# Optimization experiments

Hardware: AMD Instinct MI355X
Metric: run time of the kernel (lower is better)

## Reference

```python
import jax, jax.numpy as jnp
import numpy as np

HIDDEN = 1024
NUM_EXPERTS = 16
TOP_K = 2
I_TEXT = 512
I_VISION = 256
NUM_SHARED = 2
NORM_MIN = 1e-12


def _sparse_moe(x, router_w, bias, gate_up, down):
    """One Ernie4_5_VLMoeSparseMoeBlock applied to flat tokens x: [T, H].

    router_w: [E, H], bias: [E] (e_score_correction_bias),
    gate_up: [E, H, 2I], down: [E, I, H].
    Returns (y [T, H], router_logits [T, E]).
    """
    T = x.shape[0]
    # fp32 router (torch runs it with autocast disabled in float32)
    logits = x @ router_w.T                                  # [T, E]
    probs = jax.nn.softmax(logits, axis=-1)
    # top-k on bias-corrected probs, but gather the *uncorrected* probs
    _, sel = jax.lax.top_k(probs + bias[None, :], TOP_K)     # [T, k]
    w = jnp.take_along_axis(probs, sel, axis=1)              # [T, k]
    w = w / jnp.maximum(jnp.sum(w, axis=-1, keepdims=True), NORM_MIN)
    # sparse combine matrix [T, E] with k nonzeros per row
    combine = jnp.zeros((T, NUM_EXPERTS), x.dtype).at[
        jnp.arange(T)[:, None], sel].add(w)
    # batched per-expert gated-SiLU MLP (dense dispatch reference)
    gu = jnp.einsum('th,ehi->eti', x, gate_up)               # [E, T, 2I]
    g, u = jnp.split(gu, 2, axis=-1)
    h = jnp.einsum('eti,eih->eth', jax.nn.silu(g) * u, down)  # [E, T, H]
    y = jnp.einsum('te,eth->th', combine, h)                 # [T, H]
    return y, logits


def setup_inputs() -> dict:
    key = jax.random.key(0)
    ks = jax.random.split(key, 16)
    s = 0.02
    B, S = 1, 1024
    return {
        'hidden_states': jax.random.normal(ks[0], (B, S, HIDDEN), jnp.float32),
        'moe_mm_token_type_ids': jax.random.randint(ks[1], (B, S), 0, 2).astype(jnp.int32),
        'text_router_weight': s * jax.random.normal(ks[2], (NUM_EXPERTS, HIDDEN), jnp.float32),
        'text_bias': s * jax.random.normal(ks[3], (NUM_EXPERTS,), jnp.float32),
        'text_gate_up': s * jax.random.normal(ks[4], (NUM_EXPERTS, HIDDEN, 2 * I_TEXT), jnp.float32),
        'text_down': s * jax.random.normal(ks[5], (NUM_EXPERTS, I_TEXT, HIDDEN), jnp.float32),
        'vision_router_weight': s * jax.random.normal(ks[6], (NUM_EXPERTS, HIDDEN), jnp.float32),
        'vision_bias': s * jax.random.normal(ks[7], (NUM_EXPERTS,), jnp.float32),
        'vision_gate_up': s * jax.random.normal(ks[8], (NUM_EXPERTS, HIDDEN, 2 * I_VISION), jnp.float32),
        'vision_down': s * jax.random.normal(ks[9], (NUM_EXPERTS, I_VISION, HIDDEN), jnp.float32),
        'shared_gate': s * jax.random.normal(ks[10], (HIDDEN, NUM_SHARED * I_TEXT), jnp.float32),
        'shared_up': s * jax.random.normal(ks[11], (HIDDEN, NUM_SHARED * I_TEXT), jnp.float32),
        'shared_down': s * jax.random.normal(ks[12], (NUM_SHARED * I_TEXT, HIDDEN), jnp.float32),
    }


def reference(hidden_states, moe_mm_token_type_ids,
              text_router_weight, text_bias, text_gate_up, text_down,
              vision_router_weight, vision_bias, vision_gate_up, vision_down,
              shared_gate, shared_up, shared_down):
    B, S, H = hidden_states.shape
    x = hidden_states.reshape(-1, H)                         # [T, H]
    # shared experts MLP (gated SiLU) on all tokens
    shared = (jax.nn.silu(x @ shared_gate) * (x @ shared_up)) @ shared_down
    # modality-isolated MoEs; each is pointwise-per-token, so running both on
    # all tokens and selecting with the mask is math-equivalent to the
    # boolean-mask dispatch in the torch code (jit-friendly, no dynamic shapes)
    y_text, lg_text = _sparse_moe(x, text_router_weight, text_bias, text_gate_up, text_down)
    y_vis, lg_vis = _sparse_moe(x, vision_router_weight, vision_bias, vision_gate_up, vision_down)
    is_vision = (moe_mm_token_type_ids.reshape(-1) != 0)[:, None]  # [T, 1]
    final = jnp.where(is_vision, y_vis, y_text) + shared
    router_logits = jnp.where(is_vision, lg_vis, lg_text)    # [T, E]
    return final.reshape(B, S, H), router_logits
```

## Files before the change

### kernel.cpp

```cpp
#include <hip/hip_runtime.h>
#include <math.h>

#define TOK  1024
#define HID  1024
#define NEXP 16

typedef __attribute__((ext_vector_type(8))) short bf16x8;
typedef __attribute__((ext_vector_type(4))) float f32x4;

#define SW_GUT 0u
#define SW_GUV 16777216u
#define SW_DNT 25165824u
#define SW_DNV 33554432u
#define SW_SG  37748736u
#define SW_SU  38797312u
#define SW_SD  39845888u
#define SW_ELEMS 40894464ull
#define WS_SMALL 6554624ull
#define WS_FAST (WS_SMALL + SW_ELEMS * 2ull)

__device__ __forceinline__ unsigned pack2(float f0, float f1) {
    union { float f; unsigned u; } a, b; a.f = f0; b.f = f1;
    return __builtin_amdgcn_perm(b.u + 0x8000u, a.u + 0x8000u, 0x07060302u);
}
__device__ __forceinline__ unsigned short f2bf(float f) {
    union { float f; unsigned u; } v; v.f = f;
    return (unsigned short)((v.u + 0x8000u) >> 16);
}
__device__ __forceinline__ f32x4 ntload4(const float* p) {
    return __builtin_nontemporal_load((const f32x4*)p);
}

__global__ void k_init(float* __restrict__ out, int* __restrict__ counts) {
    size_t i = (size_t)blockIdx.x * blockDim.x + threadIdx.x;
    ((float4*)out)[i] = make_float4(0.f, 0.f, 0.f, 0.f);
    if (blockIdx.x == 0 && threadIdx.x < 32) counts[threadIdx.x] = 0;
}

__global__ __launch_bounds__(64)
void k_router(const float* __restrict__ x, const int* __restrict__ tt,
              const float* __restrict__ rw_t, const float* __restrict__ b_t,
              const float* __restrict__ rw_v, const float* __restrict__ b_v,
              float* __restrict__ out_logits,
              int* __restrict__ counts, int* __restrict__ lists,
              float* __restrict__ wlist, unsigned short* __restrict__ Xbf)
{
    const int t = blockIdx.x;
    const int lane = threadIdx.x;
    const bool vis = (tt[t] != 0);
    const float* rw   = vis ? rw_v : rw_t;
    const float* bias = vis ? b_v  : b_t;
    const float* xr = x + (size_t)t * HID;

#pragma unroll
    for (int jj = 0; jj < 2; ++jj) {
        int j0 = jj * 512 + lane * 8;
        float4 lo = *(const float4*)(xr + j0);
        float4 hi = *(const float4*)(xr + j0 + 4);
        union { bf16x8 v; unsigned d[4]; } u;
        u.d[0] = pack2(lo.x, lo.y); u.d[1] = pack2(lo.z, lo.w);
        u.d[2] = pack2(hi.x, hi.y); u.d[3] = pack2(hi.z, hi.w);
        *(bf16x8*)(Xbf + (size_t)t * HID + j0) = u.v;
    }

    float acc[NEXP];
#pragma unroll
    for (int e = 0; e < NEXP; ++e) acc[e] = 0.f;
    for (int j = 0; j < HID; j += 64) {
        const float xv = xr[j + lane];
#pragma unroll
        for (int e = 0; e < NEXP; ++e)
            acc[e] = fmaf(xv, rw[(size_t)e * HID + j + lane], acc[e]);
    }
#pragma unroll
    for (int e = 0; e < NEXP; ++e) {
        float v = acc[e];
#pragma unroll
        for (int off = 32; off; off >>= 1) v += __shfl_xor(v, off);
        acc[e] = v;
    }
    if (lane < NEXP) out_logits[(size_t)t * NEXP + lane] = acc[lane];

    if (lane == 0) {
        float mx = acc[0];
#pragma unroll
        for (int e = 1; e < NEXP; ++e) mx = fmaxf(mx, acc[e]);
        float p[NEXP], s = 0.f;
#pragma unroll
        for (int e = 0; e < NEXP; ++e) { p[e] = expf(acc[e] - mx); s += p[e]; }
        const float inv = 1.f / s;
#pragma unroll
        for (int e = 0; e < NEXP; ++e) p[e] *= inv;

        int s1 = 0; float v1 = p[0] + bias[0];
#pragma unroll
        for (int e = 1; e < NEXP; ++e) {
            float c = p[e] + bias[e];
            if (c > v1) { v1 = c; s1 = e; }
        }
        int s2 = -1; float v2 = -1e30f;
#pragma unroll
        for (int e = 0; e < NEXP; ++e) {
            if (e == s1) continue;
            float c = p[e] + bias[e];
            if (c > v2) { v2 = c; s2 = e; }
        }
        float w1 = p[s1], w2 = p[s2];
        float sw = fmaxf(w1 + w2, 1e-12f);
        w1 /= sw; w2 /= sw;

        const int base = vis ? NEXP : 0;
        int pos1 = atomicAdd(&counts[base + s1], 1);
        lists[(base + s1) * TOK + pos1] = t * 2 + 0;
        wlist[(base + s1) * TOK + pos1] = w1;
        int pos2 = atomicAdd(&counts[base + s2], 1);
        lists[(base + s2) * TOK + pos2] = t * 2 + 1;
        wlist[(base + s2) * TOK + pos2] = w2;
    }
}

__device__ __forceinline__ void conv_decode(
    int bid,
    const float* gut, const float* guv, const float* dnt, const float* dnv,
    const float* sg, const float* su, const float* sd, unsigned short* sw,
    const float*& src, unsigned short*& dst, int& K, int& N, int& c, int& p)
{
    if (bid < 2048)      { int i = bid;        int e = i >> 7, r = i & 127; c = r >> 2; p = r & 3; K = 1024; N = 1024; src = gut + (size_t)e * 1048576; dst = sw + SW_GUT + (size_t)e * 1048576; }
    else if (bid < 3072) { int i = bid - 2048; int e = i >> 6, r = i & 63;  c = r >> 1; p = r & 1; K = 1024; N = 512;  src = guv + (size_t)e * 524288;  dst = sw + SW_GUV + (size_t)e * 524288; }
    else if (bid < 4096) { int i = bid - 3072; int e = i >> 6, r = i & 63;  c = r >> 2; p = r & 3; K = 512;  N = 1024; src = dnt + (size_t)e * 524288;  dst = sw + SW_DNT + (size_t)e * 524288; }
    else if (bid < 4608) { int i = bid - 4096; int e = i >> 5, r = i & 31;  c = r >> 2; p = r & 3; K = 256;  N = 1024; src = dnv + (size_t)e * 262144;  dst = sw + SW_DNV + (size_t)e * 262144; }
    else if (bid < 4736) { int i = bid - 4608; c = i >> 2; p = i & 3; K = 1024; N = 1024; src = sg; dst = sw + SW_SG; }
    else if (bid < 4864) { int i = bid - 4736; c = i >> 2; p = i & 3; K = 1024; N = 1024; src = su; dst = sw + SW_SU; }
    else                 { int i = bid - 4864; c = i >> 2; p = i & 3; K = 1024; N = 1024; src = sd; dst = sw + SW_SD; }
}

__global__ __launch_bounds__(256)
void k_conv(const float* __restrict__ gut, const float* __restrict__ guv,
            const float* __restrict__ dnt, const float* __restrict__ dnv,
            const float* __restrict__ sg, const float* __restrict__ su,
            const float* __restrict__ sd, unsigned short* __restrict__ sw)
{
    __shared__ unsigned ls[16 * 258];
    const int tid = threadIdx.x;
    const int b0 = blockIdx.x * 2;

    const float *sA, *sB; unsigned short *dA, *dB;
    int KA, NA, cA, pA, KB, NB, cB, pB;
    conv_decode(b0 + 0, gut, guv, dnt, dnv, sg, su, sd, sw, sA, dA, KA, NA, cA, pA);
    conv_decode(b0 + 1, gut, guv, dnt, dnv, sg, su, sd, sw, sB, dB, KB, NB, cB, pB);

    f32x4 Ra[8], Rb[8];
#pragma unroll
    for (int i = 0; i < 4; ++i) {
        int u = tid + i * 256; int kp = u >> 6, c4 = u & 63;
        const float* r0 = sA + (size_t)(cA * 32 + 2 * kp) * NA + pA * 256 + c4 * 4;
        Ra[2 * i]     = ntload4(r0);
        Ra[2 * i + 1] = ntload4(r0 + NA);
    }
#pragma unroll
    for (int i = 0; i < 4; ++i) {
        int u = tid + i * 256; int kp = u >> 6, c4 = u & 63;
        const float* r0 = sB + (size_t)(cB * 32 + 2 * kp) * NB + pB * 256 + c4 * 4;
        Rb[2 * i]     = ntload4(r0);
        Rb[2 * i + 1] = ntload4(r0 + NB);
    }

#pragma unroll
    for (int i = 0; i < 4; ++i) {
        int u = tid + i * 256; int kp = u >> 6, c4 = u & 63;
        unsigned* lp = &ls[kp * 258 + c4 * 4];
        f32x4 a = Ra[2 * i], b = Ra[2 * i + 1];
        lp[0] = pack2(a[0], b[0]); lp[1] = pack2(a[1], b[1]);
        lp[2] = pack2(a[2], b[2]); lp[3] = pack2(a[3], b[3]);
    }
    __syncthreads();
    {
        const int KC = KA >> 5;
#pragma unroll
        for (int i = 0; i < 4; ++i) {
            int u = tid + i * 256;
            int tt = u >> 6, l = u & 63;
            int q = l >> 4, lm = l & 15;
            int col = tt * 16 + lm;
            unsigned d0 = ls[(q * 4 + 0) * 258 + col];
            unsigned d1 = ls[(q * 4 + 1) * 258 + col];
            unsigned d2 = ls[(q * 4 + 2) * 258 + col];
            unsigned d3 = ls[(q * 4 + 3) * 258 + col];
            size_t off = ((size_t)((pA * 16 + tt) * KC + cA) * 64 + l) * 8;
            *(uint4*)(dA + off) = make_uint4(d0, d1, d2, d3);
        }
    }
    __syncthreads();

#pragma unroll
    for (int i = 0; i < 4; ++i) {
        int u = tid + i * 256; int kp = u >> 6, c4 = u & 63;
        unsigned* lp = &ls[kp * 258 + c4 * 4];
        f32x4 a = Rb[2 * i], b = Rb[2 * i + 1];
        lp[0] = pack2(a[0], b[0]); lp[1] = pack2(a[1], b[1]);
        lp[2] = pack2(a[2], b[2]); lp[3] = pack2(a[3], b[3]);
    }
    __syncthreads();
    {
        const int KC = KB >> 5;
#pragma unroll
        for (int i = 0; i < 4; ++i) {
            int u = tid + i * 256;
            int tt = u >> 6, l = u & 63;
            int q = l >> 4, lm = l & 15;
            int col = tt * 16 + lm;
            unsigned d0 = ls[(q * 4 + 0) * 258 + col];
            unsigned d1 = ls[(q * 4 + 1) * 258 + col];
            unsigned d2 = ls[(q * 4 + 2) * 258 + col];
            unsigned d3 = ls[(q * 4 + 3) * 258 + col];
            size_t off = ((size_t)((pB * 16 + tt) * KC + cB) * 64 + l) * 8;
            *(uint4*)(dB + off) = make_uint4(d0, d1, d2, d3);
        }
    }
}

__global__ __launch_bounds__(256)
void k_gu2(const unsigned short* __restrict__ Xbf, const unsigned short* __restrict__ sw,
           const int* __restrict__ counts, const int* __restrict__ lists,
           unsigned short* __restrict__ hbuf, unsigned short* __restrict__ hsh)
{
    const int z = blockIdx.z;
    int M, I, utile0;
    const unsigned short *gbase, *ubase;
    if (z == 32)      { M = TOK;       I = 1024; gbase = sw + SW_SG; ubase = sw + SW_SU; utile0 = 0; }
    else if (z < 16)  { M = counts[z]; I = 512;  gbase = ubase = sw + SW_GUT + (size_t)z * 1048576; utile0 = 32; }
    else              { M = counts[z]; I = 256;  gbase = ubase = sw + SW_GUV + (size_t)(z - 16) * 524288; utile0 = 16; }
    const int xI = blockIdx.x * 16, m0 = blockIdx.y * 64;
    if (xI >= I || m0 >= M) return;

    __shared__ int s_aid[64];
    const int tid = threadIdx.x;
    if (tid < 64) {
        int r = m0 + tid;
        s_aid[tid] = (z == 32) ? r : ((r < M) ? lists[z * TOK + r] : -1);
    }
    __syncthreads();

    const int w = tid >> 6, lane = tid & 63;
    const int lm = lane & 15, q = lane >> 4;

    int aidA = s_aid[w * 16 + lm];
    int tr = (z == 32) ? aidA : (aidA < 0 ? 0 : (aidA >> 1));
    const unsigned short* arow = Xbf + (size_t)tr * HID;

    const int tg = xI >> 4;
    const int tu = utile0 + tg;
    const unsigned short* pg = gbase + (size_t)tg * 32 * 512 + lane * 8;
    const unsigned short* pu = ubase + (size_t)tu * 32 * 512 + lane * 8;
    const int ko = q * 8;

    f32x4 accG = {}, accU = {};
    bf16x8 Bg[4], Bu[4], Af[4];
#pragma unroll
    for (int p = 0; p < 4; ++p) {
        Bg[p] = *(const bf16x8*)(pg + p * 512);
        Bu[p] = *(const bf16x8*)(pu + p * 512);
        Af[p] = *(const bf16x8*)(arow + p * 32 + ko);
    }
    for (int cc = 0; cc < 32; cc += 4) {
#pragma unroll
        for (int p = 0; p < 4; ++p) {
            accG = __builtin_amdgcn_mfma_f32_16x16x32_bf16(Af[p], Bg[p], accG, 0, 0, 0);
            accU = __builtin_amdgcn_mfma_f32_16x16x32_bf16(Af[p], Bu[p], accU, 0, 0, 0);
            int cp = cc + p + 4; if (cp > 31) cp = 31;
            Bg[p] = *(const bf16x8*)(pg + cp * 512);
            Bu[p] = *(const bf16x8*)(pu + cp * 512);
            Af[p] = *(const bf16x8*)(arow + cp * 32 + ko);
        }
    }

    const int i = xI + lm;
#pragma unroll
    for (int r = 0; r < 4; ++r) {
        int row = w * 16 + q * 4 + r;
        int aid = s_aid[row];
        if (aid < 0) continue;
        float g = accG[r], uu = accU[r];
        float h = g / (1.f + __expf(-g)) * uu;
        if (z == 32) hsh[(size_t)aid * 1024 + i] = f2bf(h);
        else         hbuf[(size_t)aid * 512 + i] = f2bf(h);
    }
}

__global__ __launch_bounds__(256)
void k_down2(const unsigned short* __restrict__ hbuf, const unsigned short* __restrict__ hsh,
             const unsigned short* __restrict__ sw,
             const int* __restrict__ counts, const int* __restrict__ lists,
             const float* __restrict__ wlist, float* __restrict__ out)
{
    const int z = blockIdx.z;
    int M, K;
    const unsigned short* base;
    if (z == 32)     { M = TOK;       K = 1024; base = sw + SW_SD; }
    else if (z < 16) { M = counts[z]; K = 512;  base = sw + SW_DNT + (size_t)z * 524288; }
    else             { M = counts[z]; K = 256;  base = sw + SW_DNV + (size_t)(z - 16) * 262144; }
    const int n0 = blockIdx.x * 16, m0 = blockIdx.y * 64;
    if (m0 >= M) return;

    __shared__ int s_aid[64];
    __shared__ float s_w[64];
    const int tid = threadIdx.x;
    if (tid < 64) {
        int r = m0 + tid;
        if (z == 32)    { s_aid[tid] = r; s_w[tid] = 1.f; }
        else if (r < M) { s_aid[tid] = lists[z * TOK + r]; s_w[tid] = wlist[z * TOK + r]; }
        else            { s_aid[tid] = -1; s_w[tid] = 0.f; }
    }
    __syncthreads();

    const int w = tid >> 6, lane = tid & 63;
    const int lm = lane & 15, q = lane >> 4;

    int aidA = s_aid[w * 16 + lm];
    const unsigned short* hrow = (z == 32) ? (hsh + (size_t)aidA * 1024)
                                           : (hbuf + (size_t)(aidA < 0 ? 0 : aidA) * 512);

    const int KC = K >> 5;
    const int t = blockIdx.x;
    const unsigned short* pb = base + (size_t)t * KC * 512 + lane * 8;
    const int ko = q * 8;

    f32x4 acc = {};
    bf16x8 Bt[4], Af[4];
#pragma unroll
    for (int p = 0; p < 4; ++p) {
        Bt[p] = *(const bf16x8*)(pb + p * 512);
        Af[p] = *(const bf16x8*)(hrow + p * 32 + ko);
    }
    const int last = KC - 1;
    for (int cc = 0; cc < KC; cc += 4) {
#pragma unroll
        for (int p = 0; p < 4; ++p) {
            acc = __builtin_amdgcn_mfma_f32_16x16x32_bf16(Af[p], Bt[p], acc, 0, 0, 0);
            int cp = cc + p + 4; if (cp > last) cp = last;
            Bt[p] = *(const bf16x8*)(pb + (size_t)cp * 512);
            Af[p] = *(const bf16x8*)(hrow + cp * 32 + ko);
        }
    }

    const int col = n0 + lm;
#pragma unroll
    for (int r = 0; r < 4; ++r) {
        int row = w * 16 + q * 4 + r;
        int aid = s_aid[row];
        if (aid < 0) continue;
        int tok = (z == 32) ? aid : (aid >> 1);
        atomicAdd(&out[(size_t)tok * HID + col], s_w[row] * acc[r]);
    }
}

__global__ __launch_bounds__(256)
void k_gu_fb(const unsigned short* __restrict__ Xbf,
             const float* __restrict__ gut, const float* __restrict__ guv,
             const float* __restrict__ sg, const float* __restrict__ su,
             const int* __restrict__ counts, const int* __restrict__ lists,
             unsigned short* __restrict__ hbuf, unsigned short* __restrict__ hsh)
{
    const int z = blockIdx.z;
    int M, I, str;
    const float *Wg, *Wu;
    if (z == 32) { M = TOK; I = 1024; str = 1024; Wg = sg; Wu = su; }
    else {
        M = counts[z];
        const int mod = z >> 4, e = z & 15;
        I = mod ? 256 : 512; str = 2 * I;
        const float* base = mod ? (guv + (size_t)e * HID * 512)
                                : (gut + (size_t)e * HID * 1024);
        Wg = base; Wu = base + I;
    }
    const int xI = blockIdx.x * 64;
    const int m0 = blockIdx.y * 64;
    if (xI >= I || m0 >= M) return;

    __shared__ float bs[8192];
    __shared__ int s_aid[64];
    const int tid = threadIdx.x;
    const int wid = tid >> 6, lane = tid & 63;
    const int lm = lane & 15, q = lane >> 4;

    if (tid < 64) {
        int r = m0 + tid;
        s_aid[tid] = (z == 32) ? r : ((r < M) ? lists[z * TOK + r] : -1);
    }
    __syncthreads();

    const unsigned short* arow[4];
#pragma unroll
    for (int s = 0; s < 4; ++s) {
        int aid = s_aid[s * 16 + lm];
        int tr = (z == 32) ? aid : (aid < 0 ? 0 : (aid >> 1));
        arow[s] = Xbf + (size_t)tr * HID;
    }
    int urow[8], uc4[8], scell[8];
#pragma unroll
    for (int r = 0; r < 8; ++r) {
        int u = r * 256 + tid;
        int k = u >> 5;
        urow[r] = k; uc4[r] = u & 31;
        scell[r] = k * 32 + ((u & 31) ^ (((k >> 3) & 1) << 2));
    }
    int fidx[2];
#pragma unroll
    for (int reg = 0; reg < 2; ++reg) {
        int c = reg * 64 + wid * 16 + lm;
        fidx[reg] = (q * 8) * 128 + (((c >> 2) ^ ((q & 1) << 2)) * 4 + (c & 3));
    }
    float4 R[8];
#pragma unroll
    for (int r = 0; r < 8; ++r) {
        int c4 = uc4[r];
        const float* gp = (c4 < 16) ? (Wg + (size_t)urow[r] * str + xI + c4 * 4)
                                    : (Wu + (size_t)urow[r] * str + xI + (c4 - 16) * 4);
        R[r] = *(const float4*)gp;
    }
    f32x4 accG[4] = {}, accU[4] = {};
    for (int kc = 0; kc < 16; ++kc) {
        if (kc) __syncthreads();
#pragma unroll
        for (int r = 0; r < 8; ++r)
            *(float4*)&bs[scell[r] * 4] = R[r];
        __syncthreads();
        bf16x8 af[2][4];
        const int kg = kc * 64 + q * 8;
#pragma unroll
        for (int s = 0; s < 4; ++s) {
            af[0][s] = *(const bf16x8*)(arow[s] + kg);
            af[1][s] = *(const bf16x8*)(arow[s] + kg + 32);
        }
        if (kc + 1 < 16) {
            const int k0 = (kc + 1) * 64;
#pragma unroll
            for (int r = 0; r < 8; ++r) {
                int c4 = uc4[r];
                const float* gp = (c4 < 16) ? (Wg + (size_t)(k0 + urow[r]) * str + xI + c4 * 4)
                                            : (Wu + (size_t)(k0 + urow[r]) * str + xI + (c4 - 16) * 4);
                R[r] = *(const float4*)gp;
            }
        }
#pragma unroll
        for (int ks2 = 0; ks2 < 2; ++ks2) {
            const int ks = ks2 * 32;
            bf16x8 bg, bu;
            {
                float b[8];
#pragma unroll
                for (int j = 0; j < 8; ++j) b[j] = bs[fidx[0] + (ks + j) * 128];
                union { bf16x8 v; unsigned d[4]; } u;
                u.d[0] = pack2(b[0], b[1]); u.d[1] = pack2(b[2], b[3]);
                u.d[2] = pack2(b[4], b[5]); u.d[3] = pack2(b[6], b[7]);
                bg = u.v;
            }
            {
                float b[8];
#pragma unroll
                for (int j = 0; j < 8; ++j) b[j] = bs[fidx[1] + (ks + j) * 128];
                union { bf16x8 v; unsigned d[4]; } u;
                u.d[0] = pack2(b[0], b[1]); u.d[1] = pack2(b[2], b[3]);
                u.d[2] = pack2(b[4], b[5]); u.d[3] = pack2(b[6], b[7]);
                bu = u.v;
            }
#pragma unroll
            for (int s = 0; s < 4; ++s) {
                accG[s] = __builtin_amdgcn_mfma_f32_16x16x32_bf16(af[ks2][s], bg, accG[s], 0, 0, 0);
                accU[s] = __builtin_amdgcn_mfma_f32_16x16x32_bf16(af[ks2][s], bu, accU[s], 0, 0, 0);
            }
        }
    }
    const int i = xI + wid * 16 + lm;
#pragma unroll
    for (int s = 0; s < 4; ++s)
#pragma unroll
        for (int r = 0; r < 4; ++r) {
            int row = s * 16 + q * 4 + r;
            int aid = s_aid[row];
            if (aid < 0) continue;
            float g = accG[s][r], uu = accU[s][r];
            float h = g / (1.f + __expf(-g)) * uu;
            if (z == 32) hsh[(size_t)aid * 1024 + i] = f2bf(h);
            else         hbuf[(size_t)aid * 512 + i] = f2bf(h);
        }
}

__global__ __launch_bounds__(256)
void k_down_fb(const unsigned short* __restrict__ hbuf, const unsigned short* __restrict__ hsh,
               const float* __restrict__ dnt, const float* __restrict__ dnv,
               const float* __restrict__ sd,
               const int* __restrict__ counts, const int* __restrict__ lists,
               const float* __restrict__ wlist, float* __restrict__ out)
{
    const int z = blockIdx.z;
    int M, K;
    const float* W;
    if (z == 32) { M = TOK; K = 1024; W = sd; }
    else {
        M = counts[z];
        const int mod = z >> 4, e = z & 15;
        K = mod ? 256 : 512;
        W = mod ? (dnv + (size_t)e * 256 * 1024) : (dnt + (size_t)e * 512 * 1024);
    }
    const int n0 = blockIdx.x * 128;
    const int m0 = blockIdx.y * 64;
    if (m0 >= M) return;

    __shared__ float bs[8192];
    __shared__ int s_aid[64];
    __shared__ float s_w[64];
    const int tid = threadIdx.x;
    const int wid = tid >> 6, lane = tid & 63;
    const int lm = lane & 15, q = lane >> 4;

    if (tid < 64) {
        int r = m0 + tid;
        if (z == 32)    { s_aid[tid] = r; s_w[tid] = 1.f; }
        else if (r < M) { s_aid[tid] = lists[z * TOK + r]; s_w[tid] = wlist[z * TOK + r]; }
        else            { s_aid[tid] = -1; s_w[tid] = 0.f; }
    }
    __syncthreads();

    const unsigned short* hrow[4];
#pragma unroll
    for (int s = 0; s < 4; ++s) {
        int aid = s_aid[s * 16 + lm];
        hrow[s] = (z == 32) ? (hsh + (size_t)aid * 1024)
                            : (hbuf + (size_t)(aid < 0 ? 0 : aid) * 512);
    }
    int urow[8], uc4[8], scell[8];
#pragma unroll
    for (int r = 0; r < 8; ++r) {
        int u = r * 256 + tid;
        int k = u >> 5;
        urow[r] = k; uc4[r] = u & 31;
        scell[r] = k * 32 + ((u & 31) ^ (((k >> 3) & 1) << 2));
    }
    int fidx[2];
#pragma unroll
    for (int t = 0; t < 2; ++t) {
        int c = wid * 32 + t * 16 + lm;
        fidx[t] = (q * 8) * 128 + (((c >> 2) ^ ((q & 1) << 2)) * 4 + (c & 3));
    }
    float4 R[8];
#pragma unroll
    for (int r = 0; r < 8; ++r)
        R[r] = *(const float4*)(W + (size_t)urow[r] * 1024 + n0 + uc4[r] * 4);

    f32x4 acc[4][2] = {};
    const int NC = K >> 6;
    for (int kc = 0; kc < NC; ++kc) {
        if (kc) __syncthreads();
#pragma unroll
        for (int r = 0; r < 8; ++r)
            *(float4*)&bs[scell[r] * 4] = R[r];
        __syncthreads();
        bf16x8 af[2][4];
        const int kg = kc * 64 + q * 8;
#pragma unroll
        for (int s = 0; s < 4; ++s) {
            af[0][s] = *(const bf16x8*)(hrow[s] + kg);
            af[1][s] = *(const bf16x8*)(hrow[s] + kg + 32);
        }
        if (kc + 1 < NC) {
            const int k0 = (kc + 1) * 64;
#pragma unroll
            for (int r = 0; r < 8; ++r)
                R[r] = *(const float4*)(W + (size_t)(k0 + urow[r]) * 1024 + n0 + uc4[r] * 4);
        }
#pragma unroll
        for (int ks2 = 0; ks2 < 2; ++ks2) {
            const int ks = ks2 * 32;
            bf16x8 bt[2];
#pragma unroll
            for (int t = 0; t < 2; ++t) {
                float b[8];
#pragma unroll
                for (int j = 0; j < 8; ++j) b[j] = bs[fidx[t] + (ks + j) * 128];
                union { bf16x8 v; unsigned d[4]; } u;
                u.d[0] = pack2(b[0], b[1]); u.d[1] = pack2(b[2], b[3]);
                u.d[2] = pack2(b[4], b[5]); u.d[3] = pack2(b[6], b[7]);
                bt[t] = u.v;
            }
#pragma unroll
            for (int s = 0; s < 4; ++s)
#pragma unroll
                for (int t = 0; t < 2; ++t)
                    acc[s][t] = __builtin_amdgcn_mfma_f32_16x16x32_bf16(af[ks2][s], bt[t], acc[s][t], 0, 0, 0);
        }
    }
#pragma unroll
    for (int s = 0; s < 4; ++s)
#pragma unroll
        for (int r = 0; r < 4; ++r) {
            int row = s * 16 + q * 4 + r;
            int aid = s_aid[row];
            if (aid < 0) continue;
            int tok = (z == 32) ? aid : (aid >> 1);
            float w = s_w[row];
#pragma unroll
            for (int t = 0; t < 2; ++t) {
                int col = n0 + wid * 32 + t * 16 + lm;
                atomicAdd(&out[(size_t)tok * HID + col], w * acc[s][t][r]);
            }
        }
}

extern "C" void kernel_launch(void* const* d_in, const int* in_sizes, int n_in,
                              void* d_out, int out_size, void* d_ws, size_t ws_size,
                              hipStream_t stream)
{
    const float* x    = (const float*)d_in[0];
    const int*   tt   = (const int*)d_in[1];
    const float* rw_t = (const float*)d_in[2];
    const float* b_t  = (const float*)d_in[3];
    const float* gu_t = (const float*)d_in[4];
    const float* dn_t = (const float*)d_in[5];
    const float* rw_v = (const float*)d_in[6];
    const float* b_v  = (const float*)d_in[7];
    const float* gu_v = (const float*)d_in[8];
    const float* dn_v = (const float*)d_in[9];
    const float* sg   = (const float*)d_in[10];
    const float* su   = (const float*)d_in[11];
    const float* sd   = (const float*)d_in[12];
    float* out = (float*)d_out;
    float* out_logits = out + (size_t)TOK * HID;

    char* ws = (char*)d_ws;
    int*   counts = (int*)ws;
    int*   lists  = (int*)(ws + 1024);
    float* wlist  = (float*)(ws + 1024 + 32 * TOK * 4);
    unsigned short* hbuf = (unsigned short*)(ws + 1024 + 64 * TOK * 4);
    unsigned short* hsh  = hbuf + (size_t)2048 * 512;
    unsigned short* Xbf  = hsh + (size_t)1024 * 1024;
    unsigned short* swz  = Xbf + (size_t)1024 * 1024;

    hipLaunchKernelGGL(k_init, dim3(1024), dim3(256), 0, stream, out, counts);
    hipLaunchKernelGGL(k_router, dim3(TOK), dim3(64), 0, stream,
                       x, tt, rw_t, b_t, rw_v, b_v, out_logits, counts, lists, wlist, Xbf);
    if (ws_size >= WS_FAST) {
        hipLaunchKernelGGL(k_conv, dim3(2496), dim3(256), 0, stream,
                           gu_t, gu_v, dn_t, dn_v, sg, su, sd, swz);
        hipLaunchKernelGGL(k_gu2, dim3(64, 16, 33), dim3(256), 0, stream,
                           Xbf, swz, counts, lists, hbuf, hsh);
        hipLaunchKernelGGL(k_down2, dim3(64, 16, 33), dim3(256), 0, stream,
                           hbuf, hsh, swz, counts, lists, wlist, out);
    } else {
        hipLaunchKernelGGL(k_gu_fb, dim3(16, 16, 33), dim3(256), 0, stream,
                           Xbf, gu_t, gu_v, sg, su, counts, lists, hbuf, hsh);
        hipLaunchKernelGGL(k_down_fb, dim3(8, 16, 33), dim3(256), 0, stream,
                           hbuf, hsh, dn_t, dn_v, sd, counts, lists, wlist, out);
    }
}
```

Before: 323.1 us.

## Skip bf16 pre-conversion of expert weights; read fp32 directly in GEMMs

The conversion kernel now only converts the shared-expert weights to swizzled bf16. The per-expert gate_up and down GEMMs read fp32 weights straight from the inputs and pack them to bf16 fragments in registers, with double-buffered loads. This removes a full pass that read about 100 MB of fp32 expert weights and wrote them back as bf16. In exchange, the routed GEMMs do strided scalar fp32 loads that may coalesce poorly and read the weights more than once across token tiles.

```diff
diff --git a/kernel.cpp b/kernel.cpp
--- a/kernel.cpp
+++ b/kernel.cpp
@@ -29,6 +29,12 @@
 }
 __device__ __forceinline__ f32x4 ntload4(const float* p) {
     return __builtin_nontemporal_load((const f32x4*)p);
+}
+__device__ __forceinline__ bf16x8 packfrag(const float* v) {
+    union { bf16x8 b; unsigned d[4]; } u;
+    u.d[0] = pack2(v[0], v[1]); u.d[1] = pack2(v[2], v[3]);
+    u.d[2] = pack2(v[4], v[5]); u.d[3] = pack2(v[6], v[7]);
+    return u.b;
 }
 
 __global__ void k_init(float* __restrict__ out, int* __restrict__ counts) {
@@ -119,25 +125,18 @@
     }
 }
 
-__device__ __forceinline__ void conv_decode(
-    int bid,
-    const float* gut, const float* guv, const float* dnt, const float* dnv,
-    const float* sg, const float* su, const float* sd, unsigned short* sw,
-    const float*& src, unsigned short*& dst, int& K, int& N, int& c, int& p)
+__device__ __forceinline__ void conv_decode_sh(
+    int bid, const float* sg, const float* su, const float* sd,
+    unsigned short* sw, const float*& src, unsigned short*& dst, int& c, int& p)
 {
-    if (bid < 2048)      { int i = bid;        int e = i >> 7, r = i & 127; c = r >> 2; p = r & 3; K = 1024; N = 1024; src = gut + (size_t)e * 1048576; dst = sw + SW_GUT + (size_t)e * 1048576; }
-    else if (bid < 3072) { int i = bid - 2048; int e = i >> 6, r = i & 63;  c = r >> 1; p = r & 1; K = 1024; N = 512;  src = guv + (size_t)e * 524288;  dst = sw + SW_GUV + (size_t)e * 524288; }
-    else if (bid < 4096) { int i = bid - 3072; int e = i >> 6, r = i & 63;  c = r >> 2; p = r & 3; K = 512;  N = 1024; src = dnt + (size_t)e * 524288;  dst = sw + SW_DNT + (size_t)e * 524288; }
-    else if (bid < 4608) { int i = bid - 4096; int e = i >> 5, r = i & 31;  c = r >> 2; p = r & 3; K = 256;  N = 1024; src = dnv + (size_t)e * 262144;  dst = sw + SW_DNV + (size_t)e * 262144; }
-    else if (bid < 4736) { int i = bid - 4608; c = i >> 2; p = i & 3; K = 1024; N = 1024; src = sg; dst = sw + SW_SG; }
-    else if (bid < 4864) { int i = bid - 4736; c = i >> 2; p = i & 3; K = 1024; N = 1024; src = su; dst = sw + SW_SU; }
-    else                 { int i = bid - 4864; c = i >> 2; p = i & 3; K = 1024; N = 1024; src = sd; dst = sw + SW_SD; }
+    int i = bid & 127; c = i >> 2; p = i & 3;
+    int m = bid >> 7;
+    src = (m == 0) ? sg : (m == 1) ? su : sd;
+    dst = sw + ((m == 0) ? SW_SG : (m == 1) ? SW_SU : SW_SD);
 }
 
 __global__ __launch_bounds__(256)
-void k_conv(const float* __restrict__ gut, const float* __restrict__ guv,
-            const float* __restrict__ dnt, const float* __restrict__ dnv,
-            const float* __restrict__ sg, const float* __restrict__ su,
+void k_conv(const float* __restrict__ sg, const float* __restrict__ su,
             const float* __restrict__ sd, unsigned short* __restrict__ sw)
 {
     __shared__ unsigned ls[16 * 258];
@@ -145,24 +144,24 @@
     const int b0 = blockIdx.x * 2;
 
     const float *sA, *sB; unsigned short *dA, *dB;
-    int KA, NA, cA, pA, KB, NB, cB, pB;
-    conv_decode(b0 + 0, gut, guv, dnt, dnv, sg, su, sd, sw, sA, dA, KA, NA, cA, pA);
-    conv_decode(b0 + 1, gut, guv, dnt, dnv, sg, su, sd, sw, sB, dB, KB, NB, cB, pB);
+    int cA, pA, cB, pB;
+    conv_decode_sh(b0 + 0, sg, su, sd, sw, sA, dA, cA, pA);
+    conv_decode_sh(b0 + 1, sg, su, sd, sw, sB, dB, cB, pB);
 
     f32x4 Ra[8], Rb[8];
 #pragma unroll
     for (int i = 0; i < 4; ++i) {
         int u = tid + i * 256; int kp = u >> 6, c4 = u & 63;
-        const float* r0 = sA + (size_t)(cA * 32 + 2 * kp) * NA + pA * 256 + c4 * 4;
+        const float* r0 = sA + (size_t)(cA * 32 + 2 * kp) * 1024 + pA * 256 + c4 * 4;
         Ra[2 * i]     = ntload4(r0);
-        Ra[2 * i + 1] = ntload4(r0 + NA);
+        Ra[2 * i + 1] = ntload4(r0 + 1024);
     }
 #pragma unroll
     for (int i = 0; i < 4; ++i) {
         int u = tid + i * 256; int kp = u >> 6, c4 = u & 63;
-        const float* r0 = sB + (size_t)(cB * 32 + 2 * kp) * NB + pB * 256 + c4 * 4;
+        const float* r0 = sB + (size_t)(cB * 32 + 2 * kp) * 1024 + pB * 256 + c4 * 4;
         Rb[2 * i]     = ntload4(r0);
-        Rb[2 * i + 1] = ntload4(r0 + NB);
+        Rb[2 * i + 1] = ntload4(r0 + 1024);
     }
 
 #pragma unroll
@@ -174,21 +173,18 @@
         lp[2] = pack2(a[2], b[2]); lp[3] = pack2(a[3], b[3]);
     }
     __syncthreads();
-    {
-        const int KC = KA >> 5;
-#pragma unroll
-        for (int i = 0; i < 4; ++i) {
-            int u = tid + i * 256;
-            int tt = u >> 6, l = u & 63;
-            int q = l >> 4, lm = l & 15;
-            int col = tt * 16 + lm;
-            unsigned d0 = ls[(q * 4 + 0) * 258 + col];
-            unsigned d1 = ls[(q * 4 + 1) * 258 + col];
-            unsigned d2 = ls[(q * 4 + 2) * 258 + col];
-            unsigned d3 = ls[(q * 4 + 3) * 258 + col];
-            size_t off = ((size_t)((pA * 16 + tt) * KC + cA) * 64 + l) * 8;
-            *(uint4*)(dA + off) = make_uint4(d0, d1, d2, d3);
-        }
+#pragma unroll
+    for (int i = 0; i < 4; ++i) {
+        int u = tid + i * 256;
+        int tt = u >> 6, l = u & 63;
+        int q = l >> 4, lm = l & 15;
+        int col = tt * 16 + lm;
+        unsigned d0 = ls[(q * 4 + 0) * 258 + col];
+        unsigned d1 = ls[(q * 4 + 1) * 258 + col];
+        unsigned d2 = ls[(q * 4 + 2) * 258 + col];
+        unsigned d3 = ls[(q * 4 + 3) * 258 + col];
+        size_t off = ((size_t)((pA * 16 + tt) * 32 + cA) * 64 + l) * 8;
+        *(uint4*)(dA + off) = make_uint4(d0, d1, d2, d3);
     }
     __syncthreads();
 
@@ -201,77 +197,119 @@
         lp[2] = pack2(a[2], b[2]); lp[3] = pack2(a[3], b[3]);
     }
     __syncthreads();
-    {
-        const int KC = KB >> 5;
-#pragma unroll
-        for (int i = 0; i < 4; ++i) {
-            int u = tid + i * 256;
-            int tt = u >> 6, l = u & 63;
-            int q = l >> 4, lm = l & 15;
-            int col = tt * 16 + lm;
-            unsigned d0 = ls[(q * 4 + 0) * 258 + col];
-            unsigned d1 = ls[(q * 4 + 1) * 258 + col];
-            unsigned d2 = ls[(q * 4 + 2) * 258 + col];
-            unsigned d3 = ls[(q * 4 + 3) * 258 + col];
-            size_t off = ((size_t)((pB * 16 + tt) * KC + cB) * 64 + l) * 8;
-            *(uint4*)(dB + off) = make_uint4(d0, d1, d2, d3);
-        }
+#pragma unroll
+    for (int i = 0; i < 4; ++i) {
+        int u = tid + i * 256;
+        int tt = u >> 6, l = u & 63;
+        int q = l >> 4, lm = l & 15;
+        int col = tt * 16 + lm;
+        unsigned d0 = ls[(q * 4 + 0) * 258 + col];
+        unsigned d1 = ls[(q * 4 + 1) * 258 + col];
+        unsigned d2 = ls[(q * 4 + 2) * 258 + col];
+        unsigned d3 = ls[(q * 4 + 3) * 258 + col];
+        size_t off = ((size_t)((pB * 16 + tt) * 32 + cB) * 64 + l) * 8;
+        *(uint4*)(dB + off) = make_uint4(d0, d1, d2, d3);
     }
 }
 
 __global__ __launch_bounds__(256)
-void k_gu2(const unsigned short* __restrict__ Xbf, const unsigned short* __restrict__ sw,
+void k_gu3(const unsigned short* __restrict__ Xbf,
+           const float* __restrict__ gut, const float* __restrict__ guv,
+           const unsigned short* __restrict__ sw,
            const int* __restrict__ counts, const int* __restrict__ lists,
            unsigned short* __restrict__ hbuf, unsigned short* __restrict__ hsh)
 {
     const int z = blockIdx.z;
-    int M, I, utile0;
-    const unsigned short *gbase, *ubase;
-    if (z == 32)      { M = TOK;       I = 1024; gbase = sw + SW_SG; ubase = sw + SW_SU; utile0 = 0; }
-    else if (z < 16)  { M = counts[z]; I = 512;  gbase = ubase = sw + SW_GUT + (size_t)z * 1048576; utile0 = 32; }
-    else              { M = counts[z]; I = 256;  gbase = ubase = sw + SW_GUV + (size_t)(z - 16) * 524288; utile0 = 16; }
+    const int tid = threadIdx.x;
+    const int w = tid >> 6, lane = tid & 63;
+    const int lm = lane & 15, q = lane >> 4;
+    const int ko = q * 8;
     const int xI = blockIdx.x * 16, m0 = blockIdx.y * 64;
+    __shared__ int s_aid[64];
+
+    if (z == 32) {
+        if (tid < 64) s_aid[tid] = m0 + tid;
+        __syncthreads();
+        int aidA = s_aid[w * 16 + lm];
+        const unsigned short* arow = Xbf + (size_t)aidA * HID;
+        const int tg = xI >> 4;
+        const unsigned short* pg = sw + SW_SG + (size_t)tg * 32 * 512 + lane * 8;
+        const unsigned short* pu = sw + SW_SU + (size_t)tg * 32 * 512 + lane * 8;
+        f32x4 accG = {}, accU = {};
+        bf16x8 Bg[4], Bu[4], Af[4];
+#pragma unroll
+        for (int p = 0; p < 4; ++p) {
+            Bg[p] = *(const bf16x8*)(pg + p * 512);
+            Bu[p] = *(const bf16x8*)(pu + p * 512);
+            Af[p] = *(const bf16x8*)(arow + p * 32 + ko);
+        }
+        for (int cc = 0; cc < 32; cc += 4) {
+#pragma unroll
+            for (int p = 0; p < 4; ++p) {
+                accG = __builtin_amdgcn_mfma_f32_16x16x32_bf16(Af[p], Bg[p], accG, 0, 0, 0);
+                accU = __builtin_amdgcn_mfma_f32_16x16x32_bf16(Af[p], Bu[p], accU, 0, 0, 0);
+                int cp = cc + p + 4; if (cp > 31) cp = 31;
+                Bg[p] = *(const bf16x8*)(pg + cp * 512);
+                Bu[p] = *(const bf16x8*)(pu + cp * 512);
+                Af[p] = *(const bf16x8*)(arow + cp * 32 + ko);
+            }
+        }
+        const int i = xI + lm;
+#pragma unroll
+        for (int r = 0; r < 4; ++r) {
+            int row = w * 16 + q * 4 + r;
+            int aid = s_aid[row];
+            float g = accG[r], uu = accU[r];
+            float h = g / (1.f + __expf(-g)) * uu;
+            hsh[(size_t)aid * 1024 + i] = f2bf(h);
+        }
+        return;
+    }
+
+    const int M = counts[z];
+    int I, str; const float* base;
+    if (z < 16) { I = 512; str = 1024; base = gut + (size_t)z * 1048576; }
+    else        { I = 256; str = 512;  base = guv + (size_t)(z - 16) * 524288; }
     if (xI >= I || m0 >= M) return;
 
-    __shared__ int s_aid[64];
-    const int tid = threadIdx.x;
     if (tid < 64) {
         int r = m0 + tid;
-        s_aid[tid] = (z == 32) ? r : ((r < M) ? lists[z * TOK + r] : -1);
+        s_aid[tid] = (r < M) ? lists[z * TOK + r] : -1;
     }
     __syncthreads();
 
-    const int w = tid >> 6, lane = tid & 63;
-    const int lm = lane & 15, q = lane >> 4;
-
     int aidA = s_aid[w * 16 + lm];
-    int tr = (z == 32) ? aidA : (aidA < 0 ? 0 : (aidA >> 1));
-    const unsigned short* arow = Xbf + (size_t)tr * HID;
-
-    const int tg = xI >> 4;
-    const int tu = utile0 + tg;
-    const unsigned short* pg = gbase + (size_t)tg * 32 * 512 + lane * 8;
-    const unsigned short* pu = ubase + (size_t)tu * 32 * 512 + lane * 8;
-    const int ko = q * 8;
+    const unsigned short* arow = Xbf + (size_t)(aidA < 0 ? 0 : (aidA >> 1)) * HID;
+
+    const float* pw[8];
+#pragma unroll
+    for (int j = 0; j < 8; ++j)
+        pw[j] = base + (size_t)(ko + j) * str + xI + lm;
+    const size_t cstep = (size_t)32 * str;
 
     f32x4 accG = {}, accU = {};
-    bf16x8 Bg[4], Bu[4], Af[4];
-#pragma unroll
-    for (int p = 0; p < 4; ++p) {
-        Bg[p] = *(const bf16x8*)(pg + p * 512);
-        Bu[p] = *(const bf16x8*)(pu + p * 512);
-        Af[p] = *(const bf16x8*)(arow + p * 32 + ko);
-    }
-    for (int cc = 0; cc < 32; cc += 4) {
-#pragma unroll
-        for (int p = 0; p < 4; ++p) {
-            accG = __builtin_amdgcn_mfma_f32_16x16x32_bf16(Af[p], Bg[p], accG, 0, 0, 0);
-            accU = __builtin_amdgcn_mfma_f32_16x16x32_bf16(Af[p], Bu[p], accU, 0, 0, 0);
-            int cp = cc + p + 4; if (cp > 31) cp = 31;
-            Bg[p] = *(const bf16x8*)(pg + cp * 512);
-            Bu[p] = *(const bf16x8*)(pu + cp * 512);
-            Af[p] = *(const bf16x8*)(arow + cp * 32 + ko);
-        }
+    float G0[8], U0[8], G1[8], U1[8];
+    bf16x8 A0, A1;
+#pragma unroll
+    for (int j = 0; j < 8; ++j) { G0[j] = pw[j][0]; U0[j] = pw[j][(size_t)I]; }
+    A0 = *(const bf16x8*)(arow + ko);
+    for (int c = 0; c < 32; c += 2) {
+        {
+            const size_t o = (size_t)(c + 1) * cstep;
+#pragma unroll
+            for (int j = 0; j < 8; ++j) { G1[j] = pw[j][o]; U1[j] = pw[j][o + I]; }
+            A1 = *(const bf16x8*)(arow + (c + 1) * 32 + ko);
+        }
+        accG = __builtin_amdgcn_mfma_f32_16x16x32_bf16(A0, packfrag(G0), accG, 0, 0, 0);
+        accU = __builtin_amdgcn_mfma_f32_16x16x32_bf16(A0, packfrag(U0), accU, 0, 0, 0);
+        if (c + 2 < 32) {
+            const size_t o = (size_t)(c + 2) * cstep;
+#pragma unroll
+            for (int j = 0; j < 8; ++j) { G0[j] = pw[j][o]; U0[j] = pw[j][o + I]; }
+            A0 = *(const bf16x8*)(arow + (c + 2) * 32 + ko);
+        }
+        accG = __builtin_amdgcn_mfma_f32_16x16x32_bf16(A1, packfrag(G1), accG, 0, 0, 0);
+        accU = __builtin_amdgcn_mfma_f32_16x16x32_bf16(A1, packfrag(U1), accU, 0, 0, 0);
     }
 
     const int i = xI + lm;
@@ -282,65 +320,100 @@
         if (aid < 0) continue;
         float g = accG[r], uu = accU[r];
         float h = g / (1.f + __expf(-g)) * uu;
-        if (z == 32) hsh[(size_t)aid * 1024 + i] = f2bf(h);
-        else         hbuf[(size_t)aid * 512 + i] = f2bf(h);
+        hbuf[(size_t)aid * 512 + i] = f2bf(h);
     }
 }
 
 __global__ __launch_bounds__(256)
-void k_down2(const unsigned short* __restrict__ hbuf, const unsigned short* __restrict__ hsh,
+void k_down3(const unsigned short* __restrict__ hbuf, const unsigned short* __restrict__ hsh,
+             const float* __restrict__ dnt, const float* __restrict__ dnv,
              const unsigned short* __restrict__ sw,
              const int* __restrict__ counts, const int* __restrict__ lists,
              const float* __restrict__ wlist, float* __restrict__ out)
 {
     const int z = blockIdx.z;
-    int M, K;
-    const unsigned short* base;
-    if (z == 32)     { M = TOK;       K = 1024; base = sw + SW_SD; }
-    else if (z < 16) { M = counts[z]; K = 512;  base = sw + SW_DNT + (size_t)z * 524288; }
-    else             { M = counts[z]; K = 256;  base = sw + SW_DNV + (size_t)(z - 16) * 262144; }
+    const int tid = threadIdx.x;
+    const int w = tid >> 6, lane = tid & 63;
+    const int lm = lane & 15, q = lane >> 4;
+    const int ko = q * 8;
     const int n0 = blockIdx.x * 16, m0 = blockIdx.y * 64;
-    if (m0 >= M) return;
-
     __shared__ int s_aid[64];
     __shared__ float s_w[64];
-    const int tid = threadIdx.x;
+
+    if (z == 32) {
+        if (tid < 64) s_aid[tid] = m0 + tid;
+        __syncthreads();
+        int aidA = s_aid[w * 16 + lm];
+        const unsigned short* hrow = hsh + (size_t)aidA * 1024;
+        const unsigned short* pb = sw + SW_SD + (size_t)blockIdx.x * 32 * 512 + lane * 8;
+        f32x4 acc = {};
+        bf16x8 Bt[4], Af[4];
+#pragma unroll
+        for (int p = 0; p < 4; ++p) {
+            Bt[p] = *(const bf16x8*)(pb + p * 512);
+            Af[p] = *(const bf16x8*)(hrow + p * 32 + ko);
+        }
+        for (int cc = 0; cc < 32; cc += 4) {
+#pragma unroll
+            for (int p = 0; p < 4; ++p) {
+                acc = __builtin_amdgcn_mfma_f32_16x16x32_bf16(Af[p], Bt[p], acc, 0, 0, 0);
+                int cp = cc + p + 4; if (cp > 31) cp = 31;
+                Bt[p] = *(const bf16x8*)(pb + cp * 512);
+                Af[p] = *(const bf16x8*)(hrow + cp * 32 + ko);
+            }
+        }
+        const int col = n0 + lm;
+#pragma unroll
+        for (int r = 0; r < 4; ++r) {
+            int row = w * 16 + q * 4 + r;
+            int tok = s_aid[row];
+            atomicAdd(&out[(size_t)tok * HID + col], acc[r]);
+        }
+        return;
+    }
+
+    const int M = counts[z];
+    if (m0 >= M) return;
+    int K; const float* base;
+    if (z < 16) { K = 512; base = dnt + (size_t)z * 524288; }
+    else        { K = 256; base = dnv + (size_t)(z - 16) * 262144; }
+
     if (tid < 64) {
         int r = m0 + tid;
-        if (z == 32)    { s_aid[tid] = r; s_w[tid] = 1.f; }
-        else if (r < M) { s_aid[tid] = lists[z * TOK + r]; s_w[tid] = wlist[z * TOK + r]; }
-        else            { s_aid[tid] = -1; s_w[tid] = 0.f; }
+        if (r < M) { s_aid[tid] = lists[z * TOK + r]; s_w[tid] = wlist[z * TOK + r]; }
+        else       { s_aid[tid] = -1; s_w[tid] = 0.f; }
     }
     __syncthreads();
 
-    const int w = tid >> 6, lane = tid & 63;
-    const int lm = lane & 15, q = lane >> 4;
-
     int aidA = s_aid[w * 16 + lm];
-    const unsigned short* hrow = (z == 32) ? (hsh + (size_t)aidA * 1024)
-                                           : (hbuf + (size_t)(aidA < 0 ? 0 : aidA) * 512);
-
+    const unsigned short* hrow = hbuf + (size_t)(aidA < 0 ? 0 : aidA) * 512;
+
+    const float* pw[8];
+#pragma unroll
+    for (int j = 0; j < 8; ++j)
+        pw[j] = base + (size_t)(ko + j) * 1024 + n0 + lm;
+    const size_t cstep = (size_t)32 * 1024;
     const int KC = K >> 5;
-    const int t = blockIdx.x;
-    const unsigned short* pb = base + (size_t)t * KC * 512 + lane * 8;
-    const int ko = q * 8;
 
     f32x4 acc = {};
-    bf16x8 Bt[4], Af[4];
-#pragma unroll
-    for (int p = 0; p < 4; ++p) {
-        Bt[p] = *(const bf16x8*)(pb + p * 512);
-        Af[p] = *(const bf16x8*)(hrow + p * 32 + ko);
-    }
-    const int last = KC - 1;
-    for (int cc = 0; cc < KC; cc += 4) {
-#pragma unroll
-        for (int p = 0; p < 4; ++p) {
-            acc = __builtin_amdgcn_mfma_f32_16x16x32_bf16(Af[p], Bt[p], acc, 0, 0, 0);
-            int cp = cc + p + 4; if (cp > last) cp = last;
-            Bt[p] = *(const bf16x8*)(pb + (size_t)cp * 512);
-            Af[p] = *(const bf16x8*)(hrow + cp * 32 + ko);
-        }
+    float B0[8], B1[8];
+    bf16x8 A0, A1;
+#pragma unroll
+    for (int j = 0; j < 8; ++j) B0[j] = pw[j][0];
+    A0 = *(const bf16x8*)(hrow + ko);
+    for (int c = 0; c < KC; c += 2) {
+        const size_t o1 = (size_t)(c + 1) * cstep;
+#pragma unroll
+        for (int j = 0; j < 8; ++j) B1[j] = pw[j][o1];
+        A1 = *(const bf16x8*)(hrow + (c + 1) * 32 + ko);
+        acc = __builtin_amdgcn_mfma_f32_16x16x32_bf16(A0, packfrag(B0), acc, 0, 0, 0);
+        if (c + 2 < KC) {
+            const size_t o2 = (size_t)(c + 2) * cstep;
+#pragma unroll
+            for (int j = 0; j < 8; ++j) B0[j] = pw[j][o2];
+            A0 = *(const bf16x8*)(hrow + (c + 2) * 32 + ko);
+        }
+        acc = __builtin_amdgcn_mfma_f32_16x16x32_bf16(A1, packfrag(B1), acc, 0, 0, 0);
     }
 
     const int col = n0 + lm;
@@ -349,8 +422,7 @@
         int row = w * 16 + q * 4 + r;
         int aid = s_aid[row];
         if (aid < 0) continue;
-        int tok = (z == 32) ? aid : (aid >> 1);
-        atomicAdd(&out[(size_t)tok * HID + col], s_w[row] * acc[r]);
+        atomicAdd(&out[(size_t)(aid >> 1) * HID + col], s_w[row] * acc[r]);
     }
 }
 
@@ -640,12 +712,12 @@
     hipLaunchKernelGGL(k_router, dim3(TOK), dim3(64), 0, stream,
                        x, tt, rw_t, b_t, rw_v, b_v, out_logits, counts, lists, wlist, Xbf);
     if (ws_size >= WS_FAST) {
-        hipLaunchKernelGGL(k_conv, dim3(2496), dim3(256), 0, stream,
-                           gu_t, gu_v, dn_t, dn_v, sg, su, sd, swz);
-        hipLaunchKernelGGL(k_gu2, dim3(64, 16, 33), dim3(256), 0, stream,
-                           Xbf, swz, counts, lists, hbuf, hsh);
-        hipLaunchKernelGGL(k_down2, dim3(64, 16, 33), dim3(256), 0, stream,
-                           hbuf, hsh, swz, counts, lists, wlist, out);
+        hipLaunchKernelGGL(k_conv, dim3(192), dim3(256), 0, stream,
+                           sg, su, sd, swz);
+        hipLaunchKernelGGL(k_gu3, dim3(64, 16, 33), dim3(256), 0, stream,
+                           Xbf, gu_t, gu_v, swz, counts, lists, hbuf, hsh);
+        hipLaunchKernelGGL(k_down3, dim3(64, 16, 33), dim3(256), 0, stream,
+                           hbuf, hsh, dn_t, dn_v, swz, counts, lists, wlist, out);
     } else {
         hipLaunchKernelGGL(k_gu_fb, dim3(16, 16, 33), dim3(256), 0, stream,
                            Xbf, gu_t, gu_v, sg, su, counts, lists, hbuf, hsh);
```

After: 388.7 us. 1.2x slower.

## Stage expert weight tiles into LDS via direct global-to-LDS loads

Applied to the files above, without the earlier changes.

The gate/up and down GEMM kernels now copy each block's full weight tile into shared memory using global_load_lds DMA, and waves read B fragments from LDS instead of each wave reloading them from global memory. The A-row prefetch is simplified to single-step double buffering. This aims to cut redundant global/L2 weight traffic across the four waves. In exchange, the large LDS footprint per block lowers occupancy, and the whole tile must land before compute starts, with no overlap.

```diff
diff --git a/kernel.cpp b/kernel.cpp
--- a/kernel.cpp
+++ b/kernel.cpp
@@ -29,6 +29,11 @@
 }
 __device__ __forceinline__ f32x4 ntload4(const float* p) {
     return __builtin_nontemporal_load((const f32x4*)p);
+}
+__device__ __forceinline__ void lds_dma16(const unsigned short* g, unsigned short* l) {
+    __builtin_amdgcn_global_load_lds(
+        (const __attribute__((address_space(1))) void*)g,
+        (__attribute__((address_space(3))) void*)l, 16, 0, 0);
 }
 
 __global__ void k_init(float* __restrict__ out, int* __restrict__ counts) {
@@ -220,7 +225,7 @@
 }
 
 __global__ __launch_bounds__(256)
-void k_gu2(const unsigned short* __restrict__ Xbf, const unsigned short* __restrict__ sw,
+void k_gu4(const unsigned short* __restrict__ Xbf, const unsigned short* __restrict__ sw,
            const int* __restrict__ counts, const int* __restrict__ lists,
            unsigned short* __restrict__ hbuf, unsigned short* __restrict__ hsh)
 {
@@ -233,45 +238,42 @@
     const int xI = blockIdx.x * 16, m0 = blockIdx.y * 64;
     if (xI >= I || m0 >= M) return;
 
+    __shared__ unsigned short lsB[32768];
     __shared__ int s_aid[64];
     const int tid = threadIdx.x;
+    const int w = tid >> 6, lane = tid & 63;
+
+    const int tg = xI >> 4;
+    const unsigned short* gsrc = gbase + (size_t)tg * 16384;
+    const unsigned short* usrc = ubase + (size_t)(utile0 + tg) * 16384;
+    for (int c = w; c < 32; c += 4) {
+        lds_dma16(gsrc + ((size_t)c * 64 + lane) * 8, &lsB[c * 512]);
+        lds_dma16(usrc + ((size_t)c * 64 + lane) * 8, &lsB[16384 + c * 512]);
+    }
     if (tid < 64) {
         int r = m0 + tid;
         s_aid[tid] = (z == 32) ? r : ((r < M) ? lists[z * TOK + r] : -1);
     }
     __syncthreads();
 
-    const int w = tid >> 6, lane = tid & 63;
-    const int lm = lane & 15, q = lane >> 4;
-
+    const int lm = lane & 15, q = lane >> 4, ko = q * 8;
     int aidA = s_aid[w * 16 + lm];
     int tr = (z == 32) ? aidA : (aidA < 0 ? 0 : (aidA >> 1));
     const unsigned short* arow = Xbf + (size_t)tr * HID;
 
-    const int tg = xI >> 4;
-    const int tu = utile0 + tg;
-    const unsigned short* pg = gbase + (size_t)tg * 32 * 512 + lane * 8;
-    const unsigned short* pu = ubase + (size_t)tu * 32 * 512 + lane * 8;
-    const int ko = q * 8;
-
     f32x4 accG = {}, accU = {};
-    bf16x8 Bg[4], Bu[4], Af[4];
-#pragma unroll
-    for (int p = 0; p < 4; ++p) {
-        Bg[p] = *(const bf16x8*)(pg + p * 512);
-        Bu[p] = *(const bf16x8*)(pu + p * 512);
-        Af[p] = *(const bf16x8*)(arow + p * 32 + ko);
-    }
-    for (int cc = 0; cc < 32; cc += 4) {
-#pragma unroll
-        for (int p = 0; p < 4; ++p) {
-            accG = __builtin_amdgcn_mfma_f32_16x16x32_bf16(Af[p], Bg[p], accG, 0, 0, 0);
-            accU = __builtin_amdgcn_mfma_f32_16x16x32_bf16(Af[p], Bu[p], accU, 0, 0, 0);
-            int cp = cc + p + 4; if (cp > 31) cp = 31;
-            Bg[p] = *(const bf16x8*)(pg + cp * 512);
-            Bu[p] = *(const bf16x8*)(pu + cp * 512);
-            Af[p] = *(const bf16x8*)(arow + cp * 32 + ko);
-        }
+    bf16x8 A0 = *(const bf16x8*)(arow + ko);
+    const unsigned short* lg = &lsB[lane * 8];
+    const unsigned short* lu = &lsB[16384 + lane * 8];
+#pragma unroll 8
+    for (int c = 0; c < 32; ++c) {
+        bf16x8 bg = *(const bf16x8*)(lg + c * 512);
+        bf16x8 bu = *(const bf16x8*)(lu + c * 512);
+        bf16x8 An = A0;
+        if (c + 1 < 32) An = *(const bf16x8*)(arow + (c + 1) * 32 + ko);
+        accG = __builtin_amdgcn_mfma_f32_16x16x32_bf16(A0, bg, accG, 0, 0, 0);
+        accU = __builtin_amdgcn_mfma_f32_16x16x32_bf16(A0, bu, accU, 0, 0, 0);
+        A0 = An;
     }
 
     const int i = xI + lm;
@@ -288,7 +290,7 @@
 }
 
 __global__ __launch_bounds__(256)
-void k_down2(const unsigned short* __restrict__ hbuf, const unsigned short* __restrict__ hsh,
+void k_down4(const unsigned short* __restrict__ hbuf, const unsigned short* __restrict__ hsh,
              const unsigned short* __restrict__ sw,
              const int* __restrict__ counts, const int* __restrict__ lists,
              const float* __restrict__ wlist, float* __restrict__ out)
@@ -302,9 +304,17 @@
     const int n0 = blockIdx.x * 16, m0 = blockIdx.y * 64;
     if (m0 >= M) return;
 
+    __shared__ unsigned short lsB[16384];
     __shared__ int s_aid[64];
     __shared__ float s_w[64];
     const int tid = threadIdx.x;
+    const int w = tid >> 6, lane = tid & 63;
+    const int KC = K >> 5;
+
+    const unsigned short* src = base + (size_t)blockIdx.x * KC * 512;
+    for (int c = w; c < KC; c += 4)
+        lds_dma16(src + ((size_t)c * 64 + lane) * 8, &lsB[c * 512]);
+
     if (tid < 64) {
         int r = m0 + tid;
         if (z == 32)    { s_aid[tid] = r; s_w[tid] = 1.f; }
@@ -313,34 +323,20 @@
     }
     __syncthreads();
 
-    const int w = tid >> 6, lane = tid & 63;
-    const int lm = lane & 15, q = lane >> 4;
-
+    const int lm = lane & 15, q = lane >> 4, ko = q * 8;
     int aidA = s_aid[w * 16 + lm];
     const unsigned short* hrow = (z == 32) ? (hsh + (size_t)aidA * 1024)
                                            : (hbuf + (size_t)(aidA < 0 ? 0 : aidA) * 512);
 
-    const int KC = K >> 5;
-    const int t = blockIdx.x;
-    const unsigned short* pb = base + (size_t)t * KC * 512 + lane * 8;
-    const int ko = q * 8;
-
     f32x4 acc = {};
-    bf16x8 Bt[4], Af[4];
-#pragma unroll
-    for (int p = 0; p < 4; ++p) {
-        Bt[p] = *(const bf16x8*)(pb + p * 512);
-        Af[p] = *(const bf16x8*)(hrow + p * 32 + ko);
-    }
-    const int last = KC - 1;
-    for (int cc = 0; cc < KC; cc += 4) {
-#pragma unroll
-        for (int p = 0; p < 4; ++p) {
-            acc = __builtin_amdgcn_mfma_f32_16x16x32_bf16(Af[p], Bt[p], acc, 0, 0, 0);
-            int cp = cc + p + 4; if (cp > last) cp = last;
-            Bt[p] = *(const bf16x8*)(pb + (size_t)cp * 512);
-            Af[p] = *(const bf16x8*)(hrow + cp * 32 + ko);
-        }
+    bf16x8 A0 = *(const bf16x8*)(hrow + ko);
+    const unsigned short* lb = &lsB[lane * 8];
+    for (int c = 0; c < KC; ++c) {
+        bf16x8 bt = *(const bf16x8*)(lb + c * 512);
+        bf16x8 An = A0;
+        if (c + 1 < KC) An = *(const bf16x8*)(hrow + (c + 1) * 32 + ko);
+        acc = __builtin_amdgcn_mfma_f32_16x16x32_bf16(A0, bt, acc, 0, 0, 0);
+        A0 = An;
     }
 
     const int col = n0 + lm;
@@ -642,9 +638,9 @@
     if (ws_size >= WS_FAST) {
         hipLaunchKernelGGL(k_conv, dim3(2496), dim3(256), 0, stream,
                            gu_t, gu_v, dn_t, dn_v, sg, su, sd, swz);
-        hipLaunchKernelGGL(k_gu2, dim3(64, 16, 33), dim3(256), 0, stream,
+        hipLaunchKernelGGL(k_gu4, dim3(64, 16, 33), dim3(256), 0, stream,
                            Xbf, swz, counts, lists, hbuf, hsh);
-        hipLaunchKernelGGL(k_down2, dim3(64, 16, 33), dim3(256), 0, stream,
+        hipLaunchKernelGGL(k_down4, dim3(64, 16, 33), dim3(256), 0, stream,
                            hbuf, hsh, swz, counts, lists, wlist, out);
     } else {
         hipLaunchKernelGGL(k_gu_fb, dim3(16, 16, 33), dim3(256), 0, stream,
```

Result: faster. 308.4 us (-4.6%).
